# Kernel tuning notes

Hardware: AMD Instinct MI355X
Metric: run time of the kernel (lower is better)

## Reference

```python
import jax, jax.numpy as jnp
import numpy as np

B, T, S = 64, 128, 128
E, H, D, K = 512, 1024, 1024, 1024  # embed, hidden, decoder_size, encoder.output_size
IN2 = 2 * D + 2 * H  # output_rnn input size


def gru_cell(x, h, Wih, Whh, bih, bhh):
    # PyTorch GRUCell math; gate order (r, z, n)
    gi = x @ Wih.T + bih
    gh = h @ Whh.T + bhh
    i_r, i_z, i_n = jnp.split(gi, 3, axis=-1)
    h_r, h_z, h_n = jnp.split(gh, 3, axis=-1)
    r = jax.nn.sigmoid(i_r + h_r)
    z = jax.nn.sigmoid(i_z + h_z)
    n = jnp.tanh(i_n + r * h_n)
    return (1.0 - z) * n + z * h


def setup_inputs() -> dict:
    key = jax.random.key(0)
    ks = jax.random.split(key, 24)
    p = 0.05
    rn = lambda k, s, sc=1.0: jax.random.normal(k, s, jnp.float32) * sc
    return {
        'reversed_input': rn(ks[0], (B, T, E)),
        'y_length': jnp.full((B,), T, jnp.int32),
        'mask': jnp.ones((B, T), bool),
        'y_states': rn(ks[1], (B, T, D)),
        'encoder_output': rn(ks[2], (B, S, K)),
        'src_mask': jnp.ones((B, 1, S), bool),
        # backward-reading GRU (self.rnn)
        'rnn_Wih': rn(ks[3], (3 * H, E), p), 'rnn_Whh': rn(ks[4], (3 * H, H), p),
        'rnn_bih': rn(ks[5], (3 * H,), p), 'rnn_bhh': rn(ks[6], (3 * H,), p),
        # output_rnn GRU
        'out_Wih': rn(ks[7], (3 * H, IN2), p), 'out_Whh': rn(ks[8], (3 * H, H), p),
        'out_bih': rn(ks[9], (3 * H,), p), 'out_bhh': rn(ks[10], (3 * H,), p),
        'corr_W': rn(ks[11], (D, H), p), 'corr_b': rn(ks[12], (D,), p),
        'reward_W': rn(ks[13], (2, H), p), 'reward_b': rn(ks[14], (2,), p),
        'attv_W': rn(ks[15], (H, H + K), p), 'attv_b': rn(ks[16], (H,), p),
        # Bahdanau attention (bias-free linears)
        'key_W': rn(ks[17], (H, K), p), 'query_W': rn(ks[18], (H, H), p),
        'energy_W': rn(ks[19], (1, H), p),
    }


def reference(reversed_input, y_length, mask, y_states, encoder_output, src_mask,
              rnn_Wih, rnn_Whh, rnn_bih, rnn_bhh,
              out_Wih, out_Whh, out_bih, out_bhh,
              corr_W, corr_b, reward_W, reward_b,
              attv_W, attv_b, key_W, query_W, energy_W):
    b, t, _ = reversed_input.shape
    h_dim = rnn_Whh.shape[1]
    d_dim = corr_W.shape[0]
    dt = reversed_input.dtype

    # _apply_rnn: step-by-step GRU over reversed input == full GRU scan
    def rnn_step(h, x):
        h = gru_cell(x, h, rnn_Wih, rnn_Whh, rnn_bih, rnn_bhh)
        return h, h
    h0 = jnp.zeros((b, h_dim), dt)
    _, rnn_outs = jax.lax.scan(rnn_step, h0, reversed_input.transpose(1, 0, 2))
    rnn_outputs = jnp.flip(rnn_outs.transpose(1, 0, 2), axis=1)  # [B,T,H]

    proj_keys = encoder_output @ key_W.T  # [B,S,H] precomputed attention keys
    comb_states = jnp.concatenate([y_states, rnn_outputs], axis=-1)  # [B,T,D+H]
    sm = src_mask[:, 0, :]  # [B,S]

    def step(carry, comb_t):
        h, corr_prev, att_prev = carry
        inp = jnp.concatenate([comb_t, corr_prev, att_prev], axis=-1)  # [B,2D+2H]
        h = gru_cell(inp, h, out_Wih, out_Whh, out_bih, out_bhh)  # rnn_output == hidden[-1]
        corr = jnp.tanh(h @ corr_W.T + corr_b)  # corr_activation=tanh
        reward = h @ reward_W.T + reward_b  # [B,2]
        reward_pred = jax.lax.stop_gradient(jnp.argmax(reward, axis=-1)).astype(dt)[:, None]
        # Bahdanau attention: v^T tanh(Wq q + Wk k)
        pq = h @ query_W.T  # [B,H]
        energies = jnp.tanh(pq[:, None, :] + proj_keys) @ energy_W[0]  # [B,S]
        scores = jnp.where(sm, energies, -jnp.inf)
        alphas = jax.nn.softmax(scores, axis=-1)
        context = jnp.einsum('bs,bsk->bk', alphas, encoder_output)
        att_vec = jnp.tanh(jnp.concatenate([h, context], axis=-1) @ attv_W.T + attv_b)
        corr = corr * (1.0 - reward_pred)
        return (h, corr, att_vec), (corr, reward, alphas)

    init = (jnp.zeros((b, h_dim), dt), jnp.zeros((b, d_dim), dt), jnp.zeros((b, h_dim), dt))
    _, (corrs, rewards, attns) = jax.lax.scan(step, init, comb_states.transpose(1, 0, 2))
    return (corrs.transpose(1, 0, 2), rewards.transpose(1, 0, 2), attns.transpose(1, 0, 2))
```

## Files before the change

### kernel.cpp

```cpp
#include <hip/hip_runtime.h>
#include <hip/hip_bf16.h>
#include <math.h>

#define B 64
#define T 128
#define S 128
#define E 512
#define H 1024
#define D 1024
#define KDIM 1024
#define G3 3072
#define KCH 256

__device__ __forceinline__ float sigmoidf_(float x) { return 1.f / (1.f + expf(-x)); }

struct SubSeg { const float* A; const float* W; int lda; int ldw; };
struct SegArgs { SubSeg s[20]; };

__global__ __launch_bounds__(256) void seg_gemm(SegArgs args, int N, int Nstr, int colOff,
                                                float* __restrict__ part) {
  const SubSeg ss = args.s[blockIdx.y];
  const int bn = blockIdx.x * 64;
  __shared__ __align__(16) float As[16][68];
  __shared__ __align__(16) float Ws[16][68];
  const int tid = threadIdx.x;
  const int tr = tid >> 4;
  const int tc = tid & 15;
  float acc[4][4];
#pragma unroll
  for (int i = 0; i < 4; ++i)
#pragma unroll
    for (int j = 0; j < 4; ++j) acc[i][j] = 0.f;

  for (int k0 = 0; k0 < KCH; k0 += 16) {
#pragma unroll
    for (int l = 0; l < 4; ++l) {
      int i = tid + l * 256;
      int r = i >> 4, kk = i & 15;
      As[kk][r] = ss.A[(size_t)r * ss.lda + k0 + kk];
    }
#pragma unroll
    for (int l = 0; l < 4; ++l) {
      int i = tid + l * 256;
      int c = i >> 4, kk = i & 15;
      int gc = bn + c;
      Ws[kk][c] = (gc < N) ? ss.W[(size_t)gc * ss.ldw + k0 + kk] : 0.f;
    }
    __syncthreads();
#pragma unroll
    for (int kk = 0; kk < 16; ++kk) {
      float4 av = *(const float4*)&As[kk][tr * 4];
      float4 wv = *(const float4*)&Ws[kk][tc * 4];
      float a[4] = {av.x, av.y, av.z, av.w};
      float w[4] = {wv.x, wv.y, wv.z, wv.w};
#pragma unroll
      for (int i = 0; i < 4; ++i)
#pragma unroll
        for (int j = 0; j < 4; ++j)
          acc[i][j] = fmaf(a[i], w[j], acc[i][j]);
    }
    __syncthreads();
  }
  const size_t segBase = (size_t)blockIdx.y * 64;
#pragma unroll
  for (int i = 0; i < 4; ++i) {
    int r = tr * 4 + i;
#pragma unroll
    for (int j = 0; j < 4; ++j) {
      int c = bn + tc * 4 + j;
      if (c < N) part[(segBase + r) * Nstr + colOff + c] = acc[i][j];
    }
  }
}

__global__ __launch_bounds__(256) void gru_reduce(const float* __restrict__ part, int nsGi, int nsGh,
                                                  const float* __restrict__ bih,
                                                  const float* __restrict__ bhh,
                                                  float* __restrict__ hvec, int hstride,
                                                  float* __restrict__ flip_out, int t) {
  int b = blockIdx.x;
  int j = blockIdx.y * 256 + threadIdx.x;
  float gir = bih[j], giz = bih[H + j], gin = bih[2 * H + j];
  for (int s2 = 0; s2 < nsGi; ++s2) {
    const float* p = part + ((size_t)s2 * 64 + b) * G3;
    gir += p[j]; giz += p[H + j]; gin += p[2 * H + j];
  }
  float ghr = bhh[j], ghz = bhh[H + j], ghn = bhh[2 * H + j];
  for (int s2 = nsGi; s2 < nsGi + nsGh; ++s2) {
    const float* p = part + ((size_t)s2 * 64 + b) * G3;
    ghr += p[j]; ghz += p[H + j]; ghn += p[2 * H + j];
  }
  float r = sigmoidf_(gir + ghr);
  float z = sigmoidf_(giz + ghz);
  float n = tanhf(gin + r * ghn);
  float hold = hvec[(size_t)b * hstride + j];
  float hnew = (1.f - z) * n + z * hold;
  hvec[(size_t)b * hstride + j] = hnew;
  if (flip_out) flip_out[((size_t)b * T + (T - 1 - t)) * H + j] = hnew;
}

__global__ __launch_bounds__(256) void hproj_reduce(const float* __restrict__ part,
                                                    const float* __restrict__ corr_b,
                                                    const float* __restrict__ reward_b,
                                                    float* __restrict__ corrbuf,
                                                    float* __restrict__ rewards_t,
                                                    float* __restrict__ pqbuf) {
  int b = blockIdx.x;
  int n = blockIdx.y * 256 + threadIdx.x;
  if (n >= 2050) return;
  float v = 0.f;
#pragma unroll
  for (int s2 = 0; s2 < 4; ++s2) v += part[((size_t)s2 * 64 + b) * 2050 + n];
  if (n < 1024) corrbuf[b * 1024 + n] = v + corr_b[n];
  else if (n < 1026) rewards_t[(size_t)b * T * 2 + (n - 1024)] = v + reward_b[n - 1024];
  else pqbuf[b * 1024 + (n - 1026)] = v;
}

__global__ __launch_bounds__(256) void energy_kernel(const float* __restrict__ pq,
                                                     const float* __restrict__ pk,
                                                     const float* __restrict__ eW,
                                                     float* __restrict__ energies) {
  int wid = (blockIdx.x * 256 + threadIdx.x) >> 6;
  int lane = threadIdx.x & 63;
  int b = wid >> 7, s = wid & (S - 1);
  const float* pkp = pk + ((size_t)b * S + s) * H;
  const float* qp = pq + (size_t)b * H;
  float acc = 0.f;
#pragma unroll
  for (int j = lane; j < H; j += 64) acc += tanhf(qp[j] + pkp[j]) * eW[j];
#pragma unroll
  for (int off = 32; off > 0; off >>= 1) acc += __shfl_down(acc, off);
  if (lane == 0) energies[b * S + s] = acc;
}

__global__ void softmax_kernel(const float* __restrict__ energies, float* __restrict__ alphas,
                               float* __restrict__ out_attn, int t) {
  int b = blockIdx.x;
  int s = threadIdx.x;
  float v = energies[b * S + s];
  __shared__ float red[128];
  red[s] = v;
  __syncthreads();
  for (int st = 64; st > 0; st >>= 1) {
    if (s < st) red[s] = fmaxf(red[s], red[s + st]);
    __syncthreads();
  }
  float mx = red[0];
  __syncthreads();
  float e = expf(v - mx);
  red[s] = e;
  __syncthreads();
  for (int st = 64; st > 0; st >>= 1) {
    if (s < st) red[s] += red[s + st];
    __syncthreads();
  }
  float a = e / red[0];
  alphas[b * S + s] = a;
  out_attn[((size_t)b * T + t) * S + s] = a;
}

__global__ __launch_bounds__(256) void context_kernel(const float* __restrict__ alphas,
                                                      const float* __restrict__ enc,
                                                      float* __restrict__ hcat) {
  int b = blockIdx.x;
  int k = blockIdx.y * 256 + threadIdx.x;
  __shared__ float al[S];
  if (threadIdx.x < S) al[threadIdx.x] = alphas[b * S + threadIdx.x];
  __syncthreads();
  const float* eb = enc + (size_t)b * S * KDIM;
  float acc = 0.f;
#pragma unroll 4
  for (int s2 = 0; s2 < S; ++s2) acc = fmaf(al[s2], eb[(size_t)s2 * KDIM + k], acc);
  hcat[(size_t)b * 2048 + 1024 + k] = acc;
}

__global__ __launch_bounds__(256) void finalize_kernel(const float* __restrict__ corrbuf,
                                                       const float* __restrict__ partAttv,
                                                       const float* __restrict__ attv_b,
                                                       const float* __restrict__ rewards_t,
                                                       float* __restrict__ uv,
                                                       float* __restrict__ out_corrs, int t) {
  int b = blockIdx.x;
  int j = blockIdx.y * 256 + threadIdx.x;
  if (j < 1024) {
    float r0 = rewards_t[(size_t)b * T * 2 + 0];
    float r1 = rewards_t[(size_t)b * T * 2 + 1];
    float val = (r1 > r0) ? 0.f : tanhf(corrbuf[b * 1024 + j]);
    uv[(size_t)b * 2048 + j] = val;
    out_corrs[((size_t)b * T + t) * D + j] = val;
  } else {
    int n = j - 1024;
    float v = attv_b[n];
#pragma unroll
    for (int s2 = 0; s2 < 8; ++s2) v += partAttv[((size_t)s2 * 64 + b) * 1024 + n];
    uv[(size_t)b * 2048 + j] = tanhf(v);
  }
}

__global__ __launch_bounds__(256) void gemm_nt_big(const float* __restrict__ A, int sA,
                                                   const float* __restrict__ W, int sW,
                                                   float* __restrict__ C, int sC,
                                                   int M, int N, int Kd) {
  __shared__ __align__(16) float As[16][68];
  __shared__ __align__(16) float Ws[16][68];
  const int bm = blockIdx.y * 64;
  const int bn = blockIdx.x * 64;
  const int tid = threadIdx.x;
  const int tr = tid >> 4;
  const int tc = tid & 15;
  float acc[4][4];
#pragma unroll
  for (int i = 0; i < 4; ++i)
#pragma unroll
    for (int j = 0; j < 4; ++j) acc[i][j] = 0.f;
  for (int k0 = 0; k0 < Kd; k0 += 16) {
#pragma unroll
    for (int l = 0; l < 4; ++l) {
      int i = tid + l * 256;
      int r = i >> 4, kk = i & 15;
      As[kk][r] = A[(size_t)(bm + r) * sA + k0 + kk];
    }
#pragma unroll
    for (int l = 0; l < 4; ++l) {
      int i = tid + l * 256;
      int c = i >> 4, kk = i & 15;
      Ws[kk][c] = W[(size_t)(bn + c) * sW + k0 + kk];
    }
    __syncthreads();
#pragma unroll
    for (int kk = 0; kk < 16; ++kk) {
      float4 av = *(const float4*)&As[kk][tr * 4];
      float4 wv = *(const float4*)&Ws[kk][tc * 4];
      float a[4] = {av.x, av.y, av.z, av.w};
      float w[4] = {wv.x, wv.y, wv.z, wv.w};
#pragma unroll
      for (int i = 0; i < 4; ++i)
#pragma unroll
        for (int j = 0; j < 4; ++j)
          acc[i][j] = fmaf(a[i], w[j], acc[i][j]);
    }
    __syncthreads();
  }
#pragma unroll
  for (int i = 0; i < 4; ++i)
#pragma unroll
    for (int j = 0; j < 4; ++j)
      C[(size_t)(bm + tr * 4 + i) * sC + bn + tc * 4 + j] = acc[i][j];
}

extern "C" void kernel_launch(void* const* d_in, const int* in_sizes, int n_in,
                              void* d_out, int out_size, void* d_ws, size_t ws_size,
                              hipStream_t stream) {
  const float* reversed_input = (const float*)d_in[0];
  const float* y_states = (const float*)d_in[3];
  const float* encoder  = (const float*)d_in[4];
  const float* rnn_Wih = (const float*)d_in[6];
  const float* rnn_Whh = (const float*)d_in[7];
  const float* rnn_bih = (const float*)d_in[8];
  const float* rnn_bhh = (const float*)d_in[9];
  const float* out_Wih = (const float*)d_in[10];
  const float* out_Whh = (const float*)d_in[11];
  const float* out_bih = (const float*)d_in[12];
  const float* out_bhh = (const float*)d_in[13];
  const float* corr_W  = (const float*)d_in[14];
  const float* corr_b  = (const float*)d_in[15];
  const float* reward_W = (const float*)d_in[16];
  const float* reward_b = (const float*)d_in[17];
  const float* attv_W  = (const float*)d_in[18];
  const float* attv_b  = (const float*)d_in[19];
  const float* key_W   = (const float*)d_in[20];
  const float* query_W = (const float*)d_in[21];
  const float* energy_W = (const float*)d_in[22];

  float* out_corrs   = (float*)d_out;
  float* out_rewards = out_corrs + (size_t)B * T * D;
  float* out_attns   = out_rewards + (size_t)B * T * 2;

  float* p = (float*)d_ws;
  float* rnn_flip  = p; p += (size_t)B * T * H;
  float* proj_keys = p; p += (size_t)B * S * H;
  float* part      = p; p += (size_t)20 * 64 * G3;
  float* hcat  = p; p += (size_t)B * 2048;
  float* uv    = p; p += (size_t)B * 2048;
  float* h1    = p; p += (size_t)B * H;
  float* pqbuf = p; p += (size_t)B * H;
  float* corrbuf = p; p += (size_t)B * D;
  float* energies = p; p += (size_t)B * S;
  float* alphas   = p; p += (size_t)B * S;

  hipMemsetAsync(h1, 0, (size_t)B * H * sizeof(float), stream);
  hipMemsetAsync(hcat, 0, (size_t)B * 2048 * sizeof(float), stream);
  hipMemsetAsync(uv, 0, (size_t)B * 2048 * sizeof(float), stream);

  dim3 blk(256);

  gemm_nt_big<<<dim3(H / 64, (B * S) / 64), blk, 0, stream>>>(
      encoder, KDIM, key_W, KDIM, proj_keys, H, B * S, H, KDIM);

  for (int t = 0; t < T; ++t) {
    SegArgs sa{};
    int q = 0;
    for (int c = 0; c < 2; ++c) sa.s[q++] = { reversed_input + (size_t)t * E + c * KCH, rnn_Wih + c * KCH, T * E, E };
    for (int c = 0; c < 4; ++c) sa.s[q++] = { h1 + c * KCH, rnn_Whh + c * KCH, H, H };
    seg_gemm<<<dim3(G3 / 64, 6), blk, 0, stream>>>(sa, G3, G3, 0, part);
    gru_reduce<<<dim3(B, H / 256), blk, 0, stream>>>(part, 2, 4, rnn_bih, rnn_bhh, h1, H, rnn_flip, t);
  }

  for (int t = 0; t < T; ++t) {
    SegArgs k1{};
    int q = 0;
    for (int c = 0; c < 4; ++c) k1.s[q++] = { y_states + (size_t)t * D + c * KCH, out_Wih + c * KCH, T * D, 4096 };
    for (int c = 0; c < 4; ++c) k1.s[q++] = { rnn_flip + (size_t)t * H + c * KCH, out_Wih + 1024 + c * KCH, T * H, 4096 };
    for (int c = 0; c < 8; ++c) k1.s[q++] = { uv + c * KCH, out_Wih + 2048 + c * KCH, 2048, 4096 };
    for (int c = 0; c < 4; ++c) k1.s[q++] = { hcat + c * KCH, out_Whh + c * KCH, 2048, 1024 };
    seg_gemm<<<dim3(G3 / 64, 20), blk, 0, stream>>>(k1, G3, G3, 0, part);
    gru_reduce<<<dim3(B, H / 256), blk, 0, stream>>>(part, 16, 4, out_bih, out_bhh, hcat, 2048, nullptr, t);

    SegArgs kc{};
    for (int c = 0; c < 4; ++c) kc.s[c] = { hcat + c * KCH, corr_W + c * KCH, 2048, 1024 };
    seg_gemm<<<dim3(16, 4), blk, 0, stream>>>(kc, 1024, 2050, 0, part);
    SegArgs kr{};
    for (int c = 0; c < 4; ++c) kr.s[c] = { hcat + c * KCH, reward_W + c * KCH, 2048, 1024 };
    seg_gemm<<<dim3(1, 4), blk, 0, stream>>>(kr, 2, 2050, 1024, part);
    SegArgs kq{};
    for (int c = 0; c < 4; ++c) kq.s[c] = { hcat + c * KCH, query_W + c * KCH, 2048, 1024 };
    seg_gemm<<<dim3(16, 4), blk, 0, stream>>>(kq, 1024, 2050, 1026, part);
    hproj_reduce<<<dim3(B, 9), blk, 0, stream>>>(part, corr_b, reward_b, corrbuf,
                                                 out_rewards + (size_t)t * 2, pqbuf);

    energy_kernel<<<dim3(2048), blk, 0, stream>>>(pqbuf, proj_keys, energy_W, energies);
    softmax_kernel<<<dim3(B), dim3(S), 0, stream>>>(energies, alphas, out_attns, t);
    context_kernel<<<dim3(B, 4), blk, 0, stream>>>(alphas, encoder, hcat);

    SegArgs ka{};
    for (int c = 0; c < 8; ++c) ka.s[c] = { hcat + c * KCH, attv_W + c * KCH, 2048, 2048 };
    seg_gemm<<<dim3(16, 8), blk, 0, stream>>>(ka, 1024, 1024, 0, part);

    finalize_kernel<<<dim3(B, 8), blk, 0, stream>>>(corrbuf, part, attv_b,
                                                    out_rewards + (size_t)t * 2, uv, out_corrs, t);
  }
}
```

Before: 27.91 ms.

## Hoist input-gate GEMMs out of recurrence and use register-resident skinny GEMM

Input-side gate projections for both GRUs (reversed input, y_states and rnn output) are now computed in large chunked batched GEMMs before the per-step loop, so each step only handles the recurrent and feedback terms. The per-step tiled seg_gemm is replaced by a skinny GEMM that keeps a 128-wide slice of the 64-row activation in registers and streams weight rows, with fewer K splits. Softmax and context are fused into one kernel, and the partial buffers use a transposed layout. This trades more workspace and register pressure for fewer launches, fewer redundant weight passes and less per-step work.

```diff
diff --git a/kernel.cpp b/kernel.cpp
--- a/kernel.cpp
+++ b/kernel.cpp
@@ -10,204 +10,285 @@
 #define D 1024
 #define KDIM 1024
 #define G3 3072
-#define KCH 256
+#define JT 16
 
 __device__ __forceinline__ float sigmoidf_(float x) { return 1.f / (1.f + expf(-x)); }
 
-struct SubSeg { const float* A; const float* W; int lda; int ldw; };
-struct SegArgs { SubSeg s[20]; };
-
-__global__ __launch_bounds__(256) void seg_gemm(SegArgs args, int N, int Nstr, int colOff,
-                                                float* __restrict__ part) {
-  const SubSeg ss = args.s[blockIdx.y];
+struct SBSeg { const float* A; const float* W; int lda; int ldw; int N; int colOff; };
+struct SBArgs { SBSeg s[6]; };
+
+__global__ __launch_bounds__(256) void sb_gemm(SBArgs args, int jtPerSeg, int Nstr,
+                                               float* __restrict__ part) {
+  const int seg = blockIdx.x / jtPerSeg;
+  const int jt = blockIdx.x % jtPerSeg;
+  const SBSeg sg = args.s[seg];
+  const int j0 = jt * JT;
+  if (j0 >= sg.N) return;
+  const int wv = __builtin_amdgcn_readfirstlane(threadIdx.x >> 6);
+  const int lane = threadIdx.x & 63;
+
+  float a[128];
+  const float4* ap = (const float4*)(sg.A + (size_t)lane * sg.lda + wv * 128);
+#pragma unroll
+  for (int q = 0; q < 32; ++q) {
+    float4 v = ap[q];
+    a[q * 4 + 0] = v.x; a[q * 4 + 1] = v.y; a[q * 4 + 2] = v.z; a[q * 4 + 3] = v.w;
+  }
+  float acc[JT];
+#pragma unroll
+  for (int jj = 0; jj < JT; ++jj) acc[jj] = 0.f;
+#pragma unroll
+  for (int jj = 0; jj < JT; ++jj) {
+    int j = j0 + jj;
+    if (j < sg.N) {
+      const float4* wp = (const float4*)(sg.W + (size_t)j * sg.ldw + wv * 128);
+      float s0 = 0.f, s1 = 0.f, s2 = 0.f, s3 = 0.f;
+#pragma unroll
+      for (int q = 0; q < 32; ++q) {
+        float4 w4 = wp[q];
+        s0 = fmaf(a[q * 4 + 0], w4.x, s0);
+        s1 = fmaf(a[q * 4 + 1], w4.y, s1);
+        s2 = fmaf(a[q * 4 + 2], w4.z, s2);
+        s3 = fmaf(a[q * 4 + 3], w4.w, s3);
+      }
+      acc[jj] = (s0 + s1) + (s2 + s3);
+    }
+  }
+  __shared__ float red[4][JT][64];
+#pragma unroll
+  for (int jj = 0; jj < JT; ++jj) red[wv][jj][lane] = acc[jj];
+  __syncthreads();
+  for (int idx = threadIdx.x; idx < JT * 64; idx += 256) {
+    int jj = idx >> 6, b = idx & 63;
+    int j = j0 + jj;
+    if (j < sg.N) {
+      float v = red[0][jj][b] + red[1][jj][b] + red[2][jj][b] + red[3][jj][b];
+      part[((size_t)seg * Nstr + sg.colOff + j) * 64 + b] = v;
+    }
+  }
+}
+
+__global__ __launch_bounds__(256) void gru_reduce(
+    const float* __restrict__ part, const float* __restrict__ pre_t,
+    int giPlanes, int ghStart, int ghPlanes, const float* __restrict__ bhh,
+    float* __restrict__ hrow, int hstride, float* __restrict__ flip_out, int t) {
+  const int j0 = blockIdx.x * 4;
+  const int jj = threadIdx.x >> 6;
+  const int b = threadIdx.x & 63;
+  const int j = j0 + jj;
+  float gir = pre_t[(size_t)j * 64 + b];
+  float giz = pre_t[(size_t)(H + j) * 64 + b];
+  float gin = pre_t[(size_t)(2 * H + j) * 64 + b];
+  for (int p2 = 0; p2 < giPlanes; ++p2) {
+    const float* pp = part + (size_t)p2 * G3 * 64;
+    gir += pp[(size_t)j * 64 + b];
+    giz += pp[(size_t)(H + j) * 64 + b];
+    gin += pp[(size_t)(2 * H + j) * 64 + b];
+  }
+  float ghr = bhh[j], ghz = bhh[H + j], ghn = bhh[2 * H + j];
+  for (int p2 = ghStart; p2 < ghStart + ghPlanes; ++p2) {
+    const float* pp = part + (size_t)p2 * G3 * 64;
+    ghr += pp[(size_t)j * 64 + b];
+    ghz += pp[(size_t)(H + j) * 64 + b];
+    ghn += pp[(size_t)(2 * H + j) * 64 + b];
+  }
+  float r = sigmoidf_(gir + ghr);
+  float z = sigmoidf_(giz + ghz);
+  float n = tanhf(gin + r * ghn);
+  float hold = hrow[(size_t)b * hstride + j];
+  float hnew = (1.f - z) * n + z * hold;
+  __shared__ float st[4][64];
+  st[jj][b] = hnew;
+  __syncthreads();
+  int jl = threadIdx.x & 3, b2 = threadIdx.x >> 2;
+  float v = st[jl][b2];
+  hrow[(size_t)b2 * hstride + j0 + jl] = v;
+  if (flip_out)
+    flip_out[(size_t)b2 * T * H + (size_t)(T - 1 - t) * H + j0 + jl] = v;
+}
+
+__global__ __launch_bounds__(256) void hproj_reduce(
+    const float* __restrict__ part, const float* __restrict__ corr_b,
+    const float* __restrict__ reward_b, float* __restrict__ corrT,
+    float* __restrict__ rewT, float* __restrict__ pq,
+    float* __restrict__ out_rewards, int t) {
+  const int j0 = blockIdx.x * 4;
+  const int jj = threadIdx.x >> 6;
+  const int b = threadIdx.x & 63;
+  const int j = j0 + jj;
+  __shared__ float st[4][64];
+  float v = 0.f;
+  if (j < 2050) {
+    int p0 = (j < 1024) ? 0 : (j < 1026) ? 2 : 4;
+    v = part[((size_t)p0 * 2050 + j) * 64 + b] +
+        part[((size_t)(p0 + 1) * 2050 + j) * 64 + b];
+    if (j < 1024) {
+      corrT[(size_t)j * 64 + b] = v + corr_b[j];
+    } else if (j < 1026) {
+      int l = j - 1024;
+      float rv = v + reward_b[l];
+      rewT[l * 64 + b] = rv;
+      out_rewards[((size_t)b * T + t) * 2 + l] = rv;
+    }
+  }
+  st[jj][b] = v;
+  __syncthreads();
+  int jl = threadIdx.x & 3, b2 = threadIdx.x >> 2;
+  int jq = j0 + jl;
+  if (jq >= 1026 && jq < 2050)
+    pq[(size_t)b2 * 1024 + (jq - 1026)] = st[jl][b2];
+}
+
+__global__ __launch_bounds__(256) void energy_kernel(
+    const float* __restrict__ pq, const float* __restrict__ pk,
+    const float* __restrict__ eW, float* __restrict__ energies) {
+  int wid = blockIdx.x * 4 + (threadIdx.x >> 6);
+  int lane = threadIdx.x & 63;
+  int b = wid >> 7, s = wid & 127;
+  const float* pkp = pk + ((size_t)b * S + s) * H;
+  const float* qp = pq + (size_t)b * H;
+  float acc = 0.f;
+#pragma unroll
+  for (int i = 0; i < 16; ++i) {
+    int j = lane + i * 64;
+    acc += tanhf(qp[j] + pkp[j]) * eW[j];
+  }
+#pragma unroll
+  for (int off = 32; off > 0; off >>= 1) acc += __shfl_down(acc, off);
+  if (lane == 0) energies[b * S + s] = acc;
+}
+
+__global__ __launch_bounds__(256) void smct_kernel(
+    const float* __restrict__ energies, const float* __restrict__ enc,
+    float* __restrict__ hcat, float* __restrict__ out_attn, int t) {
+  int b = blockIdx.x, kt = blockIdx.y;
+  int tid = threadIdx.x;
+  __shared__ float se[128], sa[128], ss[128];
+  if (tid < 128) { se[tid] = energies[b * S + tid]; sa[tid] = se[tid]; }
+  __syncthreads();
+  for (int st2 = 64; st2 > 0; st2 >>= 1) {
+    if (tid < st2) sa[tid] = fmaxf(sa[tid], sa[tid + st2]);
+    __syncthreads();
+  }
+  float mx = sa[0];
+  __syncthreads();
+  if (tid < 128) { sa[tid] = expf(se[tid] - mx); ss[tid] = sa[tid]; }
+  __syncthreads();
+  for (int st2 = 64; st2 > 0; st2 >>= 1) {
+    if (tid < st2) ss[tid] += ss[tid + st2];
+    __syncthreads();
+  }
+  float inv = 1.f / ss[0];
+  __syncthreads();
+  if (tid < 128) sa[tid] *= inv;
+  __syncthreads();
+  int k = kt * 256 + tid;
+  const float* eb = enc + (size_t)b * S * KDIM;
+  float acc = 0.f;
+#pragma unroll 4
+  for (int s2 = 0; s2 < 128; ++s2) acc = fmaf(sa[s2], eb[(size_t)s2 * KDIM + k], acc);
+  hcat[(size_t)b * 2048 + 1024 + k] = acc;
+  if (kt == 0 && tid < 128) out_attn[((size_t)b * T + t) * S + tid] = sa[tid];
+}
+
+__global__ __launch_bounds__(256) void finalize_kernel(
+    const float* __restrict__ partA, const float* __restrict__ attv_b,
+    const float* __restrict__ corrT, const float* __restrict__ rewT,
+    float* __restrict__ uv, float* __restrict__ out_corrs, int t) {
+  const int j0 = blockIdx.x * 4;
+  const int jj = threadIdx.x >> 6;
+  const int b = threadIdx.x & 63;
+  const int j = j0 + jj;
+  float av = attv_b[j];
+#pragma unroll
+  for (int p2 = 0; p2 < 4; ++p2) av += partA[((size_t)p2 * 1024 + j) * 64 + b];
+  av = tanhf(av);
+  float r0 = rewT[b], r1 = rewT[64 + b];
+  float cv = (r1 > r0) ? 0.f : tanhf(corrT[(size_t)j * 64 + b]);
+  __shared__ float stA[4][64], stC[4][64];
+  stA[jj][b] = av;
+  stC[jj][b] = cv;
+  __syncthreads();
+  int jl = threadIdx.x & 3, b2 = threadIdx.x >> 2;
+  uv[(size_t)b2 * 2048 + j0 + jl] = stC[jl][b2];
+  uv[(size_t)b2 * 2048 + 1024 + j0 + jl] = stA[jl][b2];
+  out_corrs[((size_t)b2 * T + t) * D + j0 + jl] = stC[jl][b2];
+}
+
+template<int KSEL>
+__global__ __launch_bounds__(256) void gi_pre_kernel(
+    const float* __restrict__ A1, const float* __restrict__ A2,
+    const float* __restrict__ W, const float* __restrict__ bias,
+    float* __restrict__ pre, int c0) {
+  const int t = c0 + blockIdx.y;
+  const int tloc = blockIdx.y;
   const int bn = blockIdx.x * 64;
   __shared__ __align__(16) float As[16][68];
   __shared__ __align__(16) float Ws[16][68];
   const int tid = threadIdx.x;
-  const int tr = tid >> 4;
-  const int tc = tid & 15;
+  const int tr = tid >> 4, tc = tid & 15;
   float acc[4][4];
 #pragma unroll
   for (int i = 0; i < 4; ++i)
 #pragma unroll
     for (int j = 0; j < 4; ++j) acc[i][j] = 0.f;
-
-  for (int k0 = 0; k0 < KCH; k0 += 16) {
+  const int Kd = KSEL ? 2048 : 512;
+  const int ldw = KSEL ? 4096 : 512;
+  for (int k0 = 0; k0 < Kd; k0 += 16) {
 #pragma unroll
     for (int l = 0; l < 4; ++l) {
       int i = tid + l * 256;
       int r = i >> 4, kk = i & 15;
-      As[kk][r] = ss.A[(size_t)r * ss.lda + k0 + kk];
+      float va;
+      if (KSEL == 0) {
+        va = A1[(size_t)r * (T * E) + (size_t)t * E + k0 + kk];
+      } else {
+        int k = k0 + kk;
+        va = (k < 1024) ? A1[(size_t)r * (T * D) + (size_t)t * D + k]
+                        : A2[(size_t)r * (T * H) + (size_t)t * H + (k - 1024)];
+      }
+      As[kk][r] = va;
     }
 #pragma unroll
     for (int l = 0; l < 4; ++l) {
       int i = tid + l * 256;
       int c = i >> 4, kk = i & 15;
-      int gc = bn + c;
-      Ws[kk][c] = (gc < N) ? ss.W[(size_t)gc * ss.ldw + k0 + kk] : 0.f;
+      Ws[kk][c] = W[(size_t)(bn + c) * ldw + k0 + kk];
     }
     __syncthreads();
 #pragma unroll
     for (int kk = 0; kk < 16; ++kk) {
-      float4 av = *(const float4*)&As[kk][tr * 4];
-      float4 wv = *(const float4*)&Ws[kk][tc * 4];
-      float a[4] = {av.x, av.y, av.z, av.w};
-      float w[4] = {wv.x, wv.y, wv.z, wv.w};
+      float4 avv = *(const float4*)&As[kk][tr * 4];
+      float4 wvv = *(const float4*)&Ws[kk][tc * 4];
+      float aa[4] = {avv.x, avv.y, avv.z, avv.w};
+      float ww[4] = {wvv.x, wvv.y, wvv.z, wvv.w};
 #pragma unroll
       for (int i = 0; i < 4; ++i)
 #pragma unroll
         for (int j = 0; j < 4; ++j)
-          acc[i][j] = fmaf(a[i], w[j], acc[i][j]);
-    }
-    __syncthreads();
-  }
-  const size_t segBase = (size_t)blockIdx.y * 64;
-#pragma unroll
-  for (int i = 0; i < 4; ++i) {
-    int r = tr * 4 + i;
+          acc[i][j] = fmaf(aa[i], ww[j], acc[i][j]);
+    }
+    __syncthreads();
+  }
+  float* dst = pre + (size_t)tloc * G3 * 64;
+#pragma unroll
+  for (int i = 0; i < 4; ++i)
 #pragma unroll
     for (int j = 0; j < 4; ++j) {
-      int c = bn + tc * 4 + j;
-      if (c < N) part[(segBase + r) * Nstr + colOff + c] = acc[i][j];
-    }
-  }
-}
-
-__global__ __launch_bounds__(256) void gru_reduce(const float* __restrict__ part, int nsGi, int nsGh,
-                                                  const float* __restrict__ bih,
-                                                  const float* __restrict__ bhh,
-                                                  float* __restrict__ hvec, int hstride,
-                                                  float* __restrict__ flip_out, int t) {
-  int b = blockIdx.x;
-  int j = blockIdx.y * 256 + threadIdx.x;
-  float gir = bih[j], giz = bih[H + j], gin = bih[2 * H + j];
-  for (int s2 = 0; s2 < nsGi; ++s2) {
-    const float* p = part + ((size_t)s2 * 64 + b) * G3;
-    gir += p[j]; giz += p[H + j]; gin += p[2 * H + j];
-  }
-  float ghr = bhh[j], ghz = bhh[H + j], ghn = bhh[2 * H + j];
-  for (int s2 = nsGi; s2 < nsGi + nsGh; ++s2) {
-    const float* p = part + ((size_t)s2 * 64 + b) * G3;
-    ghr += p[j]; ghz += p[H + j]; ghn += p[2 * H + j];
-  }
-  float r = sigmoidf_(gir + ghr);
-  float z = sigmoidf_(giz + ghz);
-  float n = tanhf(gin + r * ghn);
-  float hold = hvec[(size_t)b * hstride + j];
-  float hnew = (1.f - z) * n + z * hold;
-  hvec[(size_t)b * hstride + j] = hnew;
-  if (flip_out) flip_out[((size_t)b * T + (T - 1 - t)) * H + j] = hnew;
-}
-
-__global__ __launch_bounds__(256) void hproj_reduce(const float* __restrict__ part,
-                                                    const float* __restrict__ corr_b,
-                                                    const float* __restrict__ reward_b,
-                                                    float* __restrict__ corrbuf,
-                                                    float* __restrict__ rewards_t,
-                                                    float* __restrict__ pqbuf) {
-  int b = blockIdx.x;
-  int n = blockIdx.y * 256 + threadIdx.x;
-  if (n >= 2050) return;
-  float v = 0.f;
-#pragma unroll
-  for (int s2 = 0; s2 < 4; ++s2) v += part[((size_t)s2 * 64 + b) * 2050 + n];
-  if (n < 1024) corrbuf[b * 1024 + n] = v + corr_b[n];
-  else if (n < 1026) rewards_t[(size_t)b * T * 2 + (n - 1024)] = v + reward_b[n - 1024];
-  else pqbuf[b * 1024 + (n - 1026)] = v;
-}
-
-__global__ __launch_bounds__(256) void energy_kernel(const float* __restrict__ pq,
-                                                     const float* __restrict__ pk,
-                                                     const float* __restrict__ eW,
-                                                     float* __restrict__ energies) {
-  int wid = (blockIdx.x * 256 + threadIdx.x) >> 6;
-  int lane = threadIdx.x & 63;
-  int b = wid >> 7, s = wid & (S - 1);
-  const float* pkp = pk + ((size_t)b * S + s) * H;
-  const float* qp = pq + (size_t)b * H;
-  float acc = 0.f;
-#pragma unroll
-  for (int j = lane; j < H; j += 64) acc += tanhf(qp[j] + pkp[j]) * eW[j];
-#pragma unroll
-  for (int off = 32; off > 0; off >>= 1) acc += __shfl_down(acc, off);
-  if (lane == 0) energies[b * S + s] = acc;
-}
-
-__global__ void softmax_kernel(const float* __restrict__ energies, float* __restrict__ alphas,
-                               float* __restrict__ out_attn, int t) {
-  int b = blockIdx.x;
-  int s = threadIdx.x;
-  float v = energies[b * S + s];
-  __shared__ float red[128];
-  red[s] = v;
-  __syncthreads();
-  for (int st = 64; st > 0; st >>= 1) {
-    if (s < st) red[s] = fmaxf(red[s], red[s + st]);
-    __syncthreads();
-  }
-  float mx = red[0];
-  __syncthreads();
-  float e = expf(v - mx);
-  red[s] = e;
-  __syncthreads();
-  for (int st = 64; st > 0; st >>= 1) {
-    if (s < st) red[s] += red[s + st];
-    __syncthreads();
-  }
-  float a = e / red[0];
-  alphas[b * S + s] = a;
-  out_attn[((size_t)b * T + t) * S + s] = a;
-}
-
-__global__ __launch_bounds__(256) void context_kernel(const float* __restrict__ alphas,
-                                                      const float* __restrict__ enc,
-                                                      float* __restrict__ hcat) {
-  int b = blockIdx.x;
-  int k = blockIdx.y * 256 + threadIdx.x;
-  __shared__ float al[S];
-  if (threadIdx.x < S) al[threadIdx.x] = alphas[b * S + threadIdx.x];
-  __syncthreads();
-  const float* eb = enc + (size_t)b * S * KDIM;
-  float acc = 0.f;
-#pragma unroll 4
-  for (int s2 = 0; s2 < S; ++s2) acc = fmaf(al[s2], eb[(size_t)s2 * KDIM + k], acc);
-  hcat[(size_t)b * 2048 + 1024 + k] = acc;
-}
-
-__global__ __launch_bounds__(256) void finalize_kernel(const float* __restrict__ corrbuf,
-                                                       const float* __restrict__ partAttv,
-                                                       const float* __restrict__ attv_b,
-                                                       const float* __restrict__ rewards_t,
-                                                       float* __restrict__ uv,
-                                                       float* __restrict__ out_corrs, int t) {
-  int b = blockIdx.x;
-  int j = blockIdx.y * 256 + threadIdx.x;
-  if (j < 1024) {
-    float r0 = rewards_t[(size_t)b * T * 2 + 0];
-    float r1 = rewards_t[(size_t)b * T * 2 + 1];
-    float val = (r1 > r0) ? 0.f : tanhf(corrbuf[b * 1024 + j]);
-    uv[(size_t)b * 2048 + j] = val;
-    out_corrs[((size_t)b * T + t) * D + j] = val;
-  } else {
-    int n = j - 1024;
-    float v = attv_b[n];
-#pragma unroll
-    for (int s2 = 0; s2 < 8; ++s2) v += partAttv[((size_t)s2 * 64 + b) * 1024 + n];
-    uv[(size_t)b * 2048 + j] = tanhf(v);
-  }
-}
-
-__global__ __launch_bounds__(256) void gemm_nt_big(const float* __restrict__ A, int sA,
-                                                   const float* __restrict__ W, int sW,
-                                                   float* __restrict__ C, int sC,
-                                                   int M, int N, int Kd) {
+      int col = bn + tc * 4 + j;
+      dst[(size_t)col * 64 + tr * 4 + i] = acc[i][j] + bias[col];
+    }
+}
+
+__global__ __launch_bounds__(256) void gemm_nt_big(
+    const float* __restrict__ A, int sA, const float* __restrict__ W, int sW,
+    float* __restrict__ C, int sC, int Kd) {
   __shared__ __align__(16) float As[16][68];
   __shared__ __align__(16) float Ws[16][68];
   const int bm = blockIdx.y * 64;
   const int bn = blockIdx.x * 64;
   const int tid = threadIdx.x;
-  const int tr = tid >> 4;
-  const int tc = tid & 15;
+  const int tr = tid >> 4, tc = tid & 15;
   float acc[4][4];
 #pragma unroll
   for (int i = 0; i < 4; ++i)
@@ -229,15 +310,15 @@
     __syncthreads();
 #pragma unroll
     for (int kk = 0; kk < 16; ++kk) {
-      float4 av = *(const float4*)&As[kk][tr * 4];
-      float4 wv = *(const float4*)&Ws[kk][tc * 4];
-      float a[4] = {av.x, av.y, av.z, av.w};
-      float w[4] = {wv.x, wv.y, wv.z, wv.w};
+      float4 avv = *(const float4*)&As[kk][tr * 4];
+      float4 wvv = *(const float4*)&Ws[kk][tc * 4];
+      float aa[4] = {avv.x, avv.y, avv.z, avv.w};
+      float ww[4] = {wvv.x, wvv.y, wvv.z, wvv.w};
 #pragma unroll
       for (int i = 0; i < 4; ++i)
 #pragma unroll
         for (int j = 0; j < 4; ++j)
-          acc[i][j] = fmaf(a[i], w[j], acc[i][j]);
+          acc[i][j] = fmaf(aa[i], ww[j], acc[i][j]);
     }
     __syncthreads();
   }
@@ -253,7 +334,7 @@
                               hipStream_t stream) {
   const float* reversed_input = (const float*)d_in[0];
   const float* y_states = (const float*)d_in[3];
-  const float* encoder  = (const float*)d_in[4];
+  const float* encoder = (const float*)d_in[4];
   const float* rnn_Wih = (const float*)d_in[6];
   const float* rnn_Whh = (const float*)d_in[7];
   const float* rnn_bih = (const float*)d_in[8];
@@ -262,31 +343,39 @@
   const float* out_Whh = (const float*)d_in[11];
   const float* out_bih = (const float*)d_in[12];
   const float* out_bhh = (const float*)d_in[13];
-  const float* corr_W  = (const float*)d_in[14];
-  const float* corr_b  = (const float*)d_in[15];
+  const float* corr_W = (const float*)d_in[14];
+  const float* corr_b = (const float*)d_in[15];
   const float* reward_W = (const float*)d_in[16];
   const float* reward_b = (const float*)d_in[17];
-  const float* attv_W  = (const float*)d_in[18];
-  const float* attv_b  = (const float*)d_in[19];
-  const float* key_W   = (const float*)d_in[20];
+  const float* attv_W = (const float*)d_in[18];
+  const float* attv_b = (const float*)d_in[19];
+  const float* key_W = (const float*)d_in[20];
   const float* query_W = (const float*)d_in[21];
   const float* energy_W = (const float*)d_in[22];
 
-  float* out_corrs   = (float*)d_out;
+  float* out_corrs = (float*)d_out;
   float* out_rewards = out_corrs + (size_t)B * T * D;
-  float* out_attns   = out_rewards + (size_t)B * T * 2;
+  float* out_attns = out_rewards + (size_t)B * T * 2;
 
   float* p = (float*)d_ws;
-  float* rnn_flip  = p; p += (size_t)B * T * H;
+  float* rnn_flip = p;  p += (size_t)B * T * H;
   float* proj_keys = p; p += (size_t)B * S * H;
-  float* part      = p; p += (size_t)20 * 64 * G3;
-  float* hcat  = p; p += (size_t)B * 2048;
-  float* uv    = p; p += (size_t)B * 2048;
-  float* h1    = p; p += (size_t)B * H;
-  float* pqbuf = p; p += (size_t)B * H;
-  float* corrbuf = p; p += (size_t)B * D;
-  float* energies = p; p += (size_t)B * S;
-  float* alphas   = p; p += (size_t)B * S;
+  float* part = p;      p += (size_t)6 * G3 * 64;
+  float* hcat = p;      p += (size_t)B * 2048;
+  float* uv = p;        p += (size_t)B * 2048;
+  float* h1 = p;        p += (size_t)B * H;
+  float* pq = p;        p += (size_t)B * H;
+  float* corrT = p;     p += (size_t)D * 64;
+  float* rewT = p;      p += 128;
+  float* energies = p;  p += (size_t)B * S;
+  size_t fixedF = (size_t)(p - (float*)d_ws);
+  int CH = 8;
+  const size_t perT = (size_t)G3 * 64;
+  if (ws_size >= (fixedF + 128ull * perT) * 4) CH = 128;
+  else if (ws_size >= (fixedF + 64ull * perT) * 4) CH = 64;
+  else if (ws_size >= (fixedF + 32ull * perT) * 4) CH = 32;
+  else if (ws_size >= (fixedF + 16ull * perT) * 4) CH = 16;
+  float* gibuf = p;
 
   hipMemsetAsync(h1, 0, (size_t)B * H * sizeof(float), stream);
   hipMemsetAsync(hcat, 0, (size_t)B * 2048 * sizeof(float), stream);
@@ -295,48 +384,53 @@
   dim3 blk(256);
 
   gemm_nt_big<<<dim3(H / 64, (B * S) / 64), blk, 0, stream>>>(
-      encoder, KDIM, key_W, KDIM, proj_keys, H, B * S, H, KDIM);
-
-  for (int t = 0; t < T; ++t) {
-    SegArgs sa{};
-    int q = 0;
-    for (int c = 0; c < 2; ++c) sa.s[q++] = { reversed_input + (size_t)t * E + c * KCH, rnn_Wih + c * KCH, T * E, E };
-    for (int c = 0; c < 4; ++c) sa.s[q++] = { h1 + c * KCH, rnn_Whh + c * KCH, H, H };
-    seg_gemm<<<dim3(G3 / 64, 6), blk, 0, stream>>>(sa, G3, G3, 0, part);
-    gru_reduce<<<dim3(B, H / 256), blk, 0, stream>>>(part, 2, 4, rnn_bih, rnn_bhh, h1, H, rnn_flip, t);
-  }
-
-  for (int t = 0; t < T; ++t) {
-    SegArgs k1{};
-    int q = 0;
-    for (int c = 0; c < 4; ++c) k1.s[q++] = { y_states + (size_t)t * D + c * KCH, out_Wih + c * KCH, T * D, 4096 };
-    for (int c = 0; c < 4; ++c) k1.s[q++] = { rnn_flip + (size_t)t * H + c * KCH, out_Wih + 1024 + c * KCH, T * H, 4096 };
-    for (int c = 0; c < 8; ++c) k1.s[q++] = { uv + c * KCH, out_Wih + 2048 + c * KCH, 2048, 4096 };
-    for (int c = 0; c < 4; ++c) k1.s[q++] = { hcat + c * KCH, out_Whh + c * KCH, 2048, 1024 };
-    seg_gemm<<<dim3(G3 / 64, 20), blk, 0, stream>>>(k1, G3, G3, 0, part);
-    gru_reduce<<<dim3(B, H / 256), blk, 0, stream>>>(part, 16, 4, out_bih, out_bhh, hcat, 2048, nullptr, t);
-
-    SegArgs kc{};
-    for (int c = 0; c < 4; ++c) kc.s[c] = { hcat + c * KCH, corr_W + c * KCH, 2048, 1024 };
-    seg_gemm<<<dim3(16, 4), blk, 0, stream>>>(kc, 1024, 2050, 0, part);
-    SegArgs kr{};
-    for (int c = 0; c < 4; ++c) kr.s[c] = { hcat + c * KCH, reward_W + c * KCH, 2048, 1024 };
-    seg_gemm<<<dim3(1, 4), blk, 0, stream>>>(kr, 2, 2050, 1024, part);
-    SegArgs kq{};
-    for (int c = 0; c < 4; ++c) kq.s[c] = { hcat + c * KCH, query_W + c * KCH, 2048, 1024 };
-    seg_gemm<<<dim3(16, 4), blk, 0, stream>>>(kq, 1024, 2050, 1026, part);
-    hproj_reduce<<<dim3(B, 9), blk, 0, stream>>>(part, corr_b, reward_b, corrbuf,
-                                                 out_rewards + (size_t)t * 2, pqbuf);
-
-    energy_kernel<<<dim3(2048), blk, 0, stream>>>(pqbuf, proj_keys, energy_W, energies);
-    softmax_kernel<<<dim3(B), dim3(S), 0, stream>>>(energies, alphas, out_attns, t);
-    context_kernel<<<dim3(B, 4), blk, 0, stream>>>(alphas, encoder, hcat);
-
-    SegArgs ka{};
-    for (int c = 0; c < 8; ++c) ka.s[c] = { hcat + c * KCH, attv_W + c * KCH, 2048, 2048 };
-    seg_gemm<<<dim3(16, 8), blk, 0, stream>>>(ka, 1024, 1024, 0, part);
-
-    finalize_kernel<<<dim3(B, 8), blk, 0, stream>>>(corrbuf, part, attv_b,
-                                                    out_rewards + (size_t)t * 2, uv, out_corrs, t);
-  }
-}
+      encoder, KDIM, key_W, KDIM, proj_keys, H, KDIM);
+
+  for (int c0 = 0; c0 < T; c0 += CH) {
+    gi_pre_kernel<0><<<dim3(G3 / 64, CH), blk, 0, stream>>>(
+        reversed_input, nullptr, rnn_Wih, rnn_bih, gibuf, c0);
+    for (int tl = 0; tl < CH; ++tl) {
+      int t = c0 + tl;
+      SBArgs s1{};
+      s1.s[0] = { h1, rnn_Whh, H, H, G3, 0 };
+      s1.s[1] = { h1 + 512, rnn_Whh + 512, H, H, G3, 0 };
+      sb_gemm<<<2 * 192, blk, 0, stream>>>(s1, 192, G3, part);
+      gru_reduce<<<256, blk, 0, stream>>>(part, gibuf + (size_t)tl * perT,
+                                          0, 0, 2, rnn_bhh, h1, H, rnn_flip, t);
+    }
+  }
+
+  for (int c0 = 0; c0 < T; c0 += CH) {
+    gi_pre_kernel<1><<<dim3(G3 / 64, CH), blk, 0, stream>>>(
+        y_states, rnn_flip, out_Wih, out_bih, gibuf, c0);
+    for (int tl = 0; tl < CH; ++tl) {
+      int t = c0 + tl;
+      SBArgs k1{};
+      for (int s2 = 0; s2 < 4; ++s2)
+        k1.s[s2] = { uv + s2 * 512, out_Wih + 2048 + s2 * 512, 2048, 4096, G3, 0 };
+      for (int s2 = 0; s2 < 2; ++s2)
+        k1.s[4 + s2] = { hcat + s2 * 512, out_Whh + s2 * 512, 2048, H, G3, 0 };
+      sb_gemm<<<6 * 192, blk, 0, stream>>>(k1, 192, G3, part);
+      gru_reduce<<<256, blk, 0, stream>>>(part, gibuf + (size_t)tl * perT,
+                                          4, 4, 2, out_bhh, hcat, 2048, nullptr, t);
+      SBArgs hp{};
+      hp.s[0] = { hcat, corr_W, 2048, H, 1024, 0 };
+      hp.s[1] = { hcat + 512, corr_W + 512, 2048, H, 1024, 0 };
+      hp.s[2] = { hcat, reward_W, 2048, H, 2, 1024 };
+      hp.s[3] = { hcat + 512, reward_W + 512, 2048, H, 2, 1024 };
+      hp.s[4] = { hcat, query_W, 2048, H, 1024, 1026 };
+      hp.s[5] = { hcat + 512, query_W + 512, 2048, H, 1024, 1026 };
+      sb_gemm<<<6 * 64, blk, 0, stream>>>(hp, 64, 2050, part);
+      hproj_reduce<<<513, blk, 0, stream>>>(part, corr_b, reward_b, corrT, rewT,
+                                            pq, out_rewards, t);
+      energy_kernel<<<2048, blk, 0, stream>>>(pq, proj_keys, energy_W, energies);
+      smct_kernel<<<dim3(B, 4), blk, 0, stream>>>(energies, encoder, hcat, out_attns, t);
+      SBArgs av{};
+      for (int s2 = 0; s2 < 4; ++s2)
+        av.s[s2] = { hcat + s2 * 512, attv_W + s2 * 512, 2048, 2048, 1024, 0 };
+      sb_gemm<<<4 * 64, blk, 0, stream>>>(av, 64, 1024, part + (size_t)6 * 2050 * 64);
+      finalize_kernel<<<256, blk, 0, stream>>>(part + (size_t)6 * 2050 * 64, attv_b,
+                                               corrT, rewT, uv, out_corrs, t);
+    }
+  }
+}
```

After: 23.32 ms. -16.4%, faster.
